# Kernel optimization log

Measured on AMD Instinct MI355X. Metric: run time of the kernel, lower is better.

## Reference

```python
import jax, jax.numpy as jnp
import numpy as np

EPS = 1e-5  # torch LayerNorm default
DT_RANK = 32  # ceil(d_model=512 / 16)


def layer_norm(x, g, b):
    mu = x.mean(-1, keepdims=True)
    var = x.var(-1, keepdims=True)
    return (x - mu) / jnp.sqrt(var + EPS) * g + b


def conv1d(x, w, b, pad):
    # x: (B, C, L), w: (O, I, K) -- torch Conv1d semantics
    y = jax.lax.conv_general_dilated(x, w, (1,), [(pad, pad)],
                                     dimension_numbers=('NCH', 'OIH', 'NCH'))
    return y + b[None, :, None]


def mamba(u, in_w, conv_w, conv_b, xproj_w, dt_w, dt_b, Alog, D, out_w, d_state, d_conv):
    # Faithful mamba_ssm Mamba block (no biases on in/x/out proj, RMS of official impl)
    Bsz, L, _ = u.shape
    xz = jnp.einsum('bld,ed->ble', u, in_w)          # (B, L, 2*Di)
    x, z = jnp.split(xz, 2, axis=-1)
    Di = x.shape[-1]
    # causal depthwise conv1d, truncated to L (padding=d_conv-1 on the left)
    xc = jax.lax.conv_general_dilated(x.transpose(0, 2, 1), conv_w[:, None, :], (1,),
                                      [(d_conv - 1, 0)],
                                      dimension_numbers=('NCH', 'OIH', 'NCH'),
                                      feature_group_count=Di)
    x = jax.nn.silu((xc + conv_b[None, :, None]).transpose(0, 2, 1))  # (B, L, Di)
    xdb = jnp.einsum('bld,ed->ble', x, xproj_w)       # (B, L, dt_rank + 2*N)
    dt = jax.nn.softplus(jnp.einsum('blr,dr->bld', xdb[..., :DT_RANK], dt_w) + dt_b)
    Bm = xdb[..., DT_RANK:DT_RANK + d_state]          # (B, L, N)
    Cm = xdb[..., DT_RANK + d_state:]                 # (B, L, N)
    A = -jnp.exp(Alog)                                # (Di, N)

    def step(h, ins):
        dt_t, x_t, B_t, C_t = ins                     # (B,Di),(B,Di),(B,N),(B,N)
        dA = jnp.exp(dt_t[..., None] * A)             # (B, Di, N)
        h = dA * h + (dt_t * x_t)[..., None] * B_t[:, None, :]
        y = (h * C_t[:, None, :]).sum(-1)             # (B, Di)
        return h, y

    h0 = jnp.zeros((Bsz, Di, d_state), u.dtype)
    xs = (dt.transpose(1, 0, 2), x.transpose(1, 0, 2),
          Bm.transpose(1, 0, 2), Cm.transpose(1, 0, 2))
    _, ys = jax.lax.scan(step, h0, xs)
    y = ys.transpose(1, 0, 2) + x * D                 # skip via D
    y = y * jax.nn.silu(z)
    return jnp.einsum('bld,od->blo', y, out_w)


def _forward(x, fe_w, fe_b, fe_ln_g, fe_ln_b, emb_ln_g, emb_ln_b,
             conv1_w, conv1_b, conv2_w, conv2_b,
             mf_in_w, mf_conv_w, mf_conv_b, mf_xproj_w, mf_dt_w, mf_dt_b, mf_Alog, mf_D, mf_out_w,
             mb_in_w, mb_conv_w, mb_conv_b, mb_xproj_w, mb_dt_w, mb_dt_b, mb_Alog, mb_D, mb_out_w,
             norm_g, norm_b, fc1_w, fc1_b, fc2_w, fc2_b):
    x = x.reshape(x.shape[0], 100, 23)
    # FrequencyEmbedding: rfft over a length-1 last dim == the signal itself; |.| then Linear+LN+ReLU
    id_mag = jnp.abs(x[..., :1])                      # (B, 100, 1)
    e = jax.nn.relu(layer_norm(id_mag @ fe_w.T + fe_b, fe_ln_g, fe_ln_b))
    id_embed = jax.nn.relu(layer_norm(e, emb_ln_g, emb_ln_b))  # outer LN+ReLU
    data = x[..., 1:].transpose(0, 2, 1)              # (B, 22, 100)
    f1 = jax.nn.relu(conv1d(data, conv1_w, conv1_b, 1))
    f2 = jax.nn.relu(conv1d(f1, conv2_w, conv2_b, 1)).transpose(0, 2, 1)  # (B,100,256)
    comb = jnp.concatenate([id_embed, f2], axis=-1)   # (B, 100, 512)
    fo = mamba(comb, mf_in_w, mf_conv_w, mf_conv_b, mf_xproj_w, mf_dt_w, mf_dt_b,
               mf_Alog, mf_D, mf_out_w, 16, 4)
    bo = mamba(comb[:, ::-1], mb_in_w, mb_conv_w, mb_conv_b, mb_xproj_w, mb_dt_w, mb_dt_b,
               mb_Alog, mb_D, mb_out_w, 8, 2)[:, ::-1]
    pooled = (fo + bo).max(axis=1)                    # (B, 512)
    pooled = layer_norm(pooled, norm_g, norm_b)       # self.norm (undefined in source; LN(512))
    h = jax.nn.relu(pooled @ fc1_w.T + fc1_b)
    return h @ fc2_w.T + fc2_b                        # (B, 4)


def setup_inputs() -> dict:
    key = jax.random.key(0)
    ks = iter(jax.random.split(key, 48))
    def n(shape, s=0.02):
        return jax.random.normal(next(ks), shape, jnp.float32) * s
    Di = 1024
    alog16 = jnp.log(jnp.tile(jnp.arange(1, 17, dtype=jnp.float32), (Di, 1)))
    alog8 = jnp.log(jnp.tile(jnp.arange(1, 9, dtype=jnp.float32), (Di, 1)))
    return {
        'x': jax.random.normal(next(ks), (512, 2300), jnp.float32),
        'fe_w': n((256, 1), 1.0), 'fe_b': jnp.zeros(256, jnp.float32),
        'fe_ln_g': jnp.ones(256, jnp.float32), 'fe_ln_b': jnp.zeros(256, jnp.float32),
        'emb_ln_g': jnp.ones(256, jnp.float32), 'emb_ln_b': jnp.zeros(256, jnp.float32),
        'conv1_w': n((128, 22, 3)), 'conv1_b': jnp.zeros(128, jnp.float32),
        'conv2_w': n((256, 128, 3)), 'conv2_b': jnp.zeros(256, jnp.float32),
        'mf_in_w': n((2 * Di, 512)), 'mf_conv_w': n((Di, 4)), 'mf_conv_b': jnp.zeros(Di, jnp.float32),
        'mf_xproj_w': n((32 + 2 * 16, Di)), 'mf_dt_w': n((Di, 32)), 'mf_dt_b': n((Di,), 0.1),
        'mf_Alog': alog16, 'mf_D': jnp.ones(Di, jnp.float32), 'mf_out_w': n((512, Di)),
        'mb_in_w': n((2 * Di, 512)), 'mb_conv_w': n((Di, 2)), 'mb_conv_b': jnp.zeros(Di, jnp.float32),
        'mb_xproj_w': n((32 + 2 * 8, Di)), 'mb_dt_w': n((Di, 32)), 'mb_dt_b': n((Di,), 0.1),
        'mb_Alog': alog8, 'mb_D': jnp.ones(Di, jnp.float32), 'mb_out_w': n((512, Di)),
        'norm_g': jnp.ones(512, jnp.float32), 'norm_b': jnp.zeros(512, jnp.float32),
        'fc1_w': n((128, 512)), 'fc1_b': jnp.zeros(128, jnp.float32),
        'fc2_w': n((4, 128)), 'fc2_b': jnp.zeros(4, jnp.float32),
    }


def reference(x, fe_w, fe_b, fe_ln_g, fe_ln_b, emb_ln_g, emb_ln_b,
              conv1_w, conv1_b, conv2_w, conv2_b,
              mf_in_w, mf_conv_w, mf_conv_b, mf_xproj_w, mf_dt_w, mf_dt_b, mf_Alog, mf_D, mf_out_w,
              mb_in_w, mb_conv_w, mb_conv_b, mb_xproj_w, mb_dt_w, mb_dt_b, mb_Alog, mb_D, mb_out_w,
              norm_g, norm_b, fc1_w, fc1_b, fc2_w, fc2_b):
    return _forward(x, fe_w, fe_b, fe_ln_g, fe_ln_b, emb_ln_g, emb_ln_b,
                    conv1_w, conv1_b, conv2_w, conv2_b,
                    mf_in_w, mf_conv_w, mf_conv_b, mf_xproj_w, mf_dt_w, mf_dt_b, mf_Alog, mf_D, mf_out_w,
                    mb_in_w, mb_conv_w, mb_conv_b, mb_xproj_w, mb_dt_w, mb_dt_b, mb_Alog, mb_D, mb_out_w,
                    norm_g, norm_b, fc1_w, fc1_b, fc2_w, fc2_b)
```

## Files before the change

kernel.cpp:

```cpp
#include <hip/hip_runtime.h>
#include <cstddef>
#include <cstdint>

#define BSZ 512
#define SEQ 100

typedef __bf16 bf16_t;
typedef __attribute__((ext_vector_type(8))) __bf16 bf16x8;
typedef __attribute__((ext_vector_type(4))) float f32x4;

__device__ __forceinline__ float sigmoidf_(float v){ return 1.f/(1.f + __expf(-v)); }
__device__ __forceinline__ float siluf_(float v){ return v * sigmoidf_(v); }
__device__ __forceinline__ float softplusf_(float v){ return (v > 20.f) ? v : __logf(1.f + __expf(v)); }

__global__ __launch_bounds__(256) void cvt_bf16_kernel(
    const float* __restrict__ src, bf16_t* __restrict__ dst, int n)
{
    int i = blockIdx.x*256 + threadIdx.x;
    if (i < n) dst[i] = (bf16_t)src[i];
}

__global__ __launch_bounds__(256) void prep_outw_kernel(
    const float* __restrict__ of, const float* __restrict__ ob, bf16_t* __restrict__ W)
{
// ... 172 lines not shown
    for (int i = 0; i < 4; ++i)
        #pragma unroll
        for (int j = 0; j < 4; ++j)
            acc[i][j] = (f32x4){0.f, 0.f, 0.f, 0.f};

    for (int k0 = 0; k0 < K; k0 += 64){
        __syncthreads();
        #pragma unroll
        for (int hh = 0; hh < 2; ++hh){
            bf16_t* Asb = hh ? As1 : As0;
            bf16_t* Wsb = hh ? Ws1 : Ws0;
            #pragma unroll
            for (int q = 0; q < 2; ++q){
                const int rt = w*32 + q*16 + rsub;
                const int lq = csub ^ ((rt >> 1) & 3);
                int ra = m0 + rt; ra = (ra < Mtot) ? ra : (Mtot - 1);
                const bf16_t* ga = A + (size_t)ra*lda + k0 + hh*32 + lq*8;
                __builtin_amdgcn_global_load_lds(
                    (const __attribute__((address_space(1))) void*)ga,
                    (__attribute__((address_space(3))) void*)&Asb[(w*32 + q*16)*32], 16, 0, 0);
                const bf16_t* gw = W + (size_t)(n0 + rt)*K + k0 + hh*32 + lq*8;
                __builtin_amdgcn_global_load_lds(
                    (const __attribute__((address_space(1))) void*)gw,
                    (__attribute__((address_space(3))) void*)&Wsb[(w*32 + q*16)*32], 16, 0, 0);
            }
        }
        __syncthreads();

        #pragma unroll
        for (int hh = 0; hh < 2; ++hh){
            bf16_t* Asb = hh ? As1 : As0;
            bf16_t* Wsb = hh ? Ws1 : Ws0;
            bf16x8 af[4], bfv[4];
            #pragma unroll
            for (int i = 0; i < 4; ++i){
                const int ra = wOffM + i*16 + col;
                af[i]  = *(const bf16x8*)&Asb[ra*32 + (quad ^ ((ra >> 1) & 3))*8];
                const int rb = wOffN + i*16 + col;
                bfv[i] = *(const bf16x8*)&Wsb[rb*32 + (quad ^ ((rb >> 1) & 3))*8];
            }
            #pragma unroll
            for (int i = 0; i < 4; ++i)
                #pragma unroll
                for (int j = 0; j < 4; ++j)
                    acc[i][j] = __builtin_amdgcn_mfma_f32_16x16x32_bf16(af[i], bfv[j], acc[i][j], 0, 0, 0);
        }
    }

    __syncthreads();
    #pragma unroll
    for (int i = 0; i < 4; ++i){
        const int row0 = wOffM + i*16 + quad*4;
        #pragma unroll
        for (int j = 0; j < 4; ++j){
            const int cT = wOffN + j*16 + col;
            #pragma unroll
            for (int r = 0; r < 4; ++r)
                smem[(row0 + r)*132 + cT] = (bf16_t)acc[i][j][r];
        }
    }
    __syncthreads();

    const int half = n0 >> 11, within = n0 & 2047;
    bf16_t* dstBase = ((within < 1024) ? xy : z) + half*1024 + (within & 1023);
    #pragma unroll
    for (int k = 0; k < 8; ++k){
        const int idx = t + k*256;
        const int row = idx >> 4;
        const int ch  = (idx & 15) * 8;
        const int gm = m0 + row;
        if (gm < Mtot)
            *(bf16x8*)&dstBase[(size_t)gm*2048 + ch] = *(const bf16x8*)&smem[row*132 + ch];
    }
}

__global__ __launch_bounds__(256) void gemm_out_kernel(
    const bf16_t* __restrict__ A, int Mtot,
    const bf16_t* __restrict__ W,
    float* __restrict__ C)
{
    __shared__ bf16_t As[2][128*32];
    __shared__ bf16_t Ws[2][128*32];
    const int t = threadIdx.x;
    const int lane = t & 63, w = t >> 6;
    const int m0 = blockIdx.x * 128, n0 = blockIdx.y * 128;
    const int rsub = lane >> 2, csub = lane & 3;
    const int col = lane & 15, quad = lane >> 4;
    const int wOffM = (w & 1) * 64, wOffN = (w >> 1) * 64;
    const int K = 2048;

    f32x4 acc[4][4];
    #pragma unroll
    for (int i = 0; i < 4; ++i)
        #pragma unroll
        for (int j = 0; j < 4; ++j)
            acc[i][j] = (f32x4){0.f, 0.f, 0.f, 0.f};

    for (int k0 = 0; k0 < K; k0 += 64){
        __syncthreads();
        #pragma unroll
        for (int hh = 0; hh < 2; ++hh){
            #pragma unroll
            for (int q = 0; q < 2; ++q){
                const int rt = w*32 + q*16 + rsub;
                const int lq = csub ^ ((rt >> 1) & 3);
                int ra = m0 + rt; ra = (ra < Mtot) ? ra : (Mtot - 1);
                const bf16_t* ga = A + (size_t)ra*K + k0 + hh*32 + lq*8;
                __builtin_amdgcn_global_load_lds(
                    (const __attribute__((address_space(1))) void*)ga,
                    (__attribute__((address_space(3))) void*)&As[hh][(w*32 + q*16)*32], 16, 0, 0);
                const bf16_t* gw = W + (size_t)(n0 + rt)*K + k0 + hh*32 + lq*8;
                __builtin_amdgcn_global_load_lds(
                    (const __attribute__((address_space(1))) void*)gw,
                    (__attribute__((address_space(3))) void*)&Ws[hh][(w*32 + q*16)*32], 16, 0, 0);
            }
        }
        __syncthreads();

        #pragma unroll
        for (int hh = 0; hh < 2; ++hh){
            bf16x8 af[4], bfv[4];
            #pragma unroll
            for (int i = 0; i < 4; ++i){
                const int ra = wOffM + i*16 + col;
                af[i]  = *(const bf16x8*)&As[hh][ra*32 + (quad ^ ((ra >> 1) & 3))*8];
                const int rb = wOffN + i*16 + col;
                bfv[i] = *(const bf16x8*)&Ws[hh][rb*32 + (quad ^ ((rb >> 1) & 3))*8];
            }
            #pragma unroll
            for (int i = 0; i < 4; ++i)
                #pragma unroll
                for (int j = 0; j < 4; ++j)
                    acc[i][j] = __builtin_amdgcn_mfma_f32_16x16x32_bf16(af[i], bfv[j], acc[i][j], 0, 0, 0);
        }
    }

    #pragma unroll
    for (int i = 0; i < 4; ++i){
        const int gmb = m0 + wOffM + i*16 + quad*4;
        #pragma unroll
        for (int j = 0; j < 4; ++j){
            const int gn = n0 + wOffN + j*16 + col;
            #pragma unroll
            for (int r = 0; r < 4; ++r){
                const int gm = gmb + r;
                if (gm < Mtot)
                    C[(size_t)gm*512 + gn] = acc[i][j][r];
            }
        }
    }
}

__global__ __launch_bounds__(256) void gemm_x_kernel(
    const bf16_t* __restrict__ xy,
    const bf16_t* __restrict__ Wf, const bf16_t* __restrict__ Wb,
    float* __restrict__ C)
{
    __shared__ bf16_t As[128*32];
    __shared__ bf16_t Ws[64*32];
    const int half = blockIdx.y;
    const bf16_t* A = xy + half*1024;
    const bf16_t* W = half ? Wb : Wf;
    const int N = half ? 48 : 64;
    const int t = threadIdx.x;
    const int lane = t & 63, w = t >> 6;
    const int m0 = blockIdx.x * 128;
    const int rsub = lane >> 2, csub = lane & 3;
    const int col = lane & 15, quad = lane >> 4;

    f32x4 acc[2][4];
    #pragma unroll
    for (int i = 0; i < 2; ++i)
        #pragma unroll
        for (int j = 0; j < 4; ++j)
            acc[i][j] = (f32x4){0.f, 0.f, 0.f, 0.f};

    for (int k0 = 0; k0 < 1024; k0 += 32){
        __syncthreads();
        #pragma unroll
        for (int q = 0; q < 2; ++q){
            const int rt = q*64 + w*16 + rsub;
            const int lq = csub ^ ((rt >> 1) & 3);
            const bf16_t* ga = A + (size_t)(m0 + rt)*2048 + k0 + lq*8;
            __builtin_amdgcn_global_load_lds(
                (const __attribute__((address_space(1))) void*)ga,
                (__attribute__((address_space(3))) void*)&As[(q*64 + w*16)*32], 16, 0, 0);
        }
        {
            const int rt = w*16 + rsub;
            const int lq = csub ^ ((rt >> 1) & 3);
            int rw = (rt < N) ? rt : (N - 1);
            const bf16_t* gw = W + (size_t)rw*1024 + k0 + lq*8;
            __builtin_amdgcn_global_load_lds(
                (const __attribute__((address_space(1))) void*)gw,
                (__attribute__((address_space(3))) void*)&Ws[(w*16)*32], 16, 0, 0);
        }
        __syncthreads();

        bf16x8 af[2], bfv[4];
        #pragma unroll
        for (int i = 0; i < 2; ++i){
            const int ra = w*32 + i*16 + col;
            af[i]  = *(const bf16x8*)&As[ra*32 + (quad ^ ((ra >> 1) & 3))*8];
        }
        #pragma unroll
        for (int j = 0; j < 4; ++j){
            const int rb = j*16 + col;
            bfv[j] = *(const bf16x8*)&Ws[rb*32 + (quad ^ ((rb >> 1) & 3))*8];
        }
        #pragma unroll
        for (int i = 0; i < 2; ++i)
            #pragma unroll
            for (int j = 0; j < 4; ++j)
                acc[i][j] = __builtin_amdgcn_mfma_f32_16x16x32_bf16(af[i], bfv[j], acc[i][j], 0, 0, 0);
    }

    #pragma unroll
    for (int i = 0; i < 2; ++i){
        const int gmb = m0 + w*32 + i*16 + quad*4;
        #pragma unroll
        for (int j = 0; j < 4; ++j){
            const int gn = j*16 + col;
            if (gn < N){
                #pragma unroll
                for (int r = 0; r < 4; ++r)
                    C[(size_t)(gmb + r)*128 + half*64 + gn] = acc[i][j][r];
            }
        }
    }
}

__global__ __launch_bounds__(256) void dt_kernel(
    const float* __restrict__ xdb,
    const float* __restrict__ dtwf, const float* __restrict__ dtbf,
    const float* __restrict__ dtwb, const float* __restrict__ dtbb,
    bf16_t* __restrict__ dtb)
{
    const int half = blockIdx.y >> 3;
    const int d = (blockIdx.y & 7)*128 + (threadIdx.x & 127);
    const int mslot = threadIdx.x >> 7;
    const int m0 = blockIdx.x * 16;
    __shared__ float sd[16*32];
    for (int i = threadIdx.x; i < 16*32; i += 256){
        int r = i >> 5, c = i & 31;
        sd[i] = xdb[(size_t)(m0 + r)*128 + half*64 + c];
    }
    const float* dw = half ? dtwb : dtwf;
    float w[32];
    #pragma unroll
    for (int r = 0; r < 32; ++r) w[r] = dw[d*32 + r];
    const float db = half ? dtbb[d] : dtbf[d];
    __syncthreads();
    #pragma unroll
    for (int i = 0; i < 8; ++i){
        const int row = mslot + i*2;
        const float* rp = &sd[row*32];
        float a = db;
        #pragma unroll
        for (int r = 0; r < 32; ++r) a += w[r]*rp[r];
        dtb[(size_t)(m0 + row)*2048 + half*1024 + d] = (bf16_t)softplusf_(a);
    }
}

template<int DC, bool REV>
__device__ __forceinline__ void conv_dev(bf16_t* base, const float* wsrc, float bias)
{
    float w[DC];
    #pragma unroll
    for (int k = 0; k < DC; ++k) w[k] = wsrc[k];
    float hist[DC-1];
    #pragma unroll
    for (int k = 0; k < DC-1; ++k) hist[k] = 0.f;
    const int step = REV ? -1 : 1;
    int l = REV ? (SEQ-1) : 0;
    for (int t0 = 0; t0 < SEQ; t0 += 10){
        float v[10];
        #pragma unroll
        for (int i = 0; i < 10; ++i) v[i] = (float)base[(size_t)(l + step*i)*2048];
        float o[10];
        #pragma unroll
        for (int i = 0; i < 10; ++i){
            float a = bias + w[DC-1]*v[i];
            #pragma unroll
            for (int j = 1; j < DC; ++j) a += w[DC-1-j]*hist[j-1];
            #pragma unroll
            for (int j = DC-2; j >= 1; --j) hist[j] = hist[j-1];
            hist[0] = v[i];
            o[i] = siluf_(a);
        }
        #pragma unroll
        for (int i = 0; i < 10; ++i)
            base[(size_t)(l + step*i)*2048] = (bf16_t)o[i];
        l += step*10;
    }
}

__global__ __launch_bounds__(256) void conv_silu_kernel(
    bf16_t* __restrict__ xy,
    const float* __restrict__ cwf, const float* __restrict__ cbf,
    const float* __restrict__ cwb, const float* __restrict__ cbb)
{
    const int gid = blockIdx.x*256 + threadIdx.x;
    const int b = gid >> 11, d2 = gid & 2047;
    const int half = d2 >> 10, d = d2 & 1023;
    bf16_t* base = xy + (size_t)b*SEQ*2048 + d2;
    if (half == 0) conv_dev<4, false>(base, cwf + d*4, cbf[d]);
    else           conv_dev<2, true >(base, cwb + d*2, cbb[d]);
}

template<int DS, bool REV, bool STRUCT>
__device__ __forceinline__ void scan_core(
    bf16_t* __restrict__ xybase, const bf16_t* __restrict__ zbase,
    const bf16_t* __restrict__ tbase, const float* __restrict__ sx,
    const float* __restrict__ Av, float Dd)
{
    float h[DS];
    #pragma unroll
    for (int s = 0; s < DS; ++s) h[s] = 0.f;
    const int step = REV ? -1 : 1;
    const float A0 = Av[0];
    int l = REV ? (SEQ-1) : 0;

    for (int t0 = 0; t0 < SEQ; t0 += 10){
        float xr[10], zr[10], tr[10];
        #pragma unroll
        for (int i = 0; i < 10; ++i){
            const size_t li = (size_t)(l + step*i);
            xr[i] = (float)xybase[li*2048];
            zr[i] = (float)zbase[li*2048];
            tr[i] = (float)tbase[li*2048];
        }
        #pragma unroll
        for (int i = 0; i < 10; ++i){
            const int li = l + step*i;
            const float4* sxl4 = (const float4*)&sx[li*2*DS];
            const float dtv = tr[i];
            const float dtx = dtv * xr[i];
            float yv = 0.f;
            if (STRUCT){
                const float r = __expf(dtv*A0);
                float rp = r;
                #pragma unroll
                for (int s4 = 0; s4 < DS/4; ++s4){
                    float4 Bv = sxl4[s4];
                    float4 Cv = sxl4[DS/4 + s4];
                    h[s4*4+0] = rp*h[s4*4+0] + dtx*Bv.x; yv += h[s4*4+0]*Cv.x; rp *= r;
                    h[s4*4+1] = rp*h[s4*4+1] + dtx*Bv.y; yv += h[s4*4+1]*Cv.y; rp *= r;
                    h[s4*4+2] = rp*h[s4*4+2] + dtx*Bv.z; yv += h[s4*4+2]*Cv.z; rp *= r;
                    h[s4*4+3] = rp*h[s4*4+3] + dtx*Bv.w; yv += h[s4*4+3]*Cv.w; rp *= r;
                }
            } else {
                #pragma unroll
                for (int s4 = 0; s4 < DS/4; ++s4){
                    float4 Bv = sxl4[s4];
                    float4 Cv = sxl4[DS/4 + s4];
                    h[s4*4+0] = __expf(dtv*Av[s4*4+0])*h[s4*4+0] + dtx*Bv.x; yv += h[s4*4+0]*Cv.x;
                    h[s4*4+1] = __expf(dtv*Av[s4*4+1])*h[s4*4+1] + dtx*Bv.y; yv += h[s4*4+1]*Cv.y;
                    h[s4*4+2] = __expf(dtv*Av[s4*4+2])*h[s4*4+2] + dtx*Bv.z; yv += h[s4*4+2]*Cv.z;
                    h[s4*4+3] = __expf(dtv*Av[s4*4+3])*h[s4*4+3] + dtx*Bv.w; yv += h[s4*4+3]*Cv.w;
                }
            }
            yv += xr[i]*Dd;
            yv *= siluf_(zr[i]);
            xybase[(size_t)li*2048] = (bf16_t)yv;
        }
        l += step*10;
    }
}

template<int DS, bool REV>
__device__ __forceinline__ void scan_dev(
    bf16_t* __restrict__ xybase, const bf16_t* __restrict__ zbase,
    const bf16_t* __restrict__ tbase, const float* __restrict__ sx,
    const float* __restrict__ Arow, float Dd)
{
    float Av[DS];
    #pragma unroll
    for (int s = 0; s < DS; ++s) Av[s] = -__expf(Arow[s]);
    bool structured = true;
    #pragma unroll
    for (int s = 1; s < DS; ++s)
        structured = structured && (fabsf(Av[s] - (float)(s+1)*Av[0]) <= 1e-4f*(float)(s+1));
    if (structured) scan_core<DS, REV, true >(xybase, zbase, tbase, sx, Av, Dd);
    else            scan_core<DS, REV, false>(xybase, zbase, tbase, sx, Av, Dd);
}

__global__ __launch_bounds__(256) void scan_kernel(
    bf16_t* __restrict__ xy, const bf16_t* __restrict__ z,
    const bf16_t* __restrict__ dtb, const float* __restrict__ xdb,
    const float* __restrict__ Alogf, const float* __restrict__ Dpf,
    const float* __restrict__ Alogb, const float* __restrict__ Dpb)
{
    const int b = blockIdx.x >> 3, s8 = blockIdx.x & 7;
    const int t = threadIdx.x;
    __shared__ float sxF[SEQ*32];
    __shared__ float sxB[SEQ*16];
    const float4* src = (const float4*)(xdb + (size_t)b*SEQ*128);

    {
        float4* dstF = (float4*)sxF;
        for (int i = t; i < SEQ*8; i += 256){
            int row = i >> 3, c = i & 7;
            dstF[row*8 + c] = src[row*32 + 8 + c];
        }
        float4* dstB = (float4*)sxB;
        for (int i = t; i < SEQ*4; i += 256){
            int row = i >> 2, c = i & 3;
            dstB[row*4 + c] = src[row*32 + 24 + c];
        }
    }
    __syncthreads();

    if (t < 128){
        const int d = s8*128 + t;
        const size_t off = (size_t)b*SEQ*2048 + d;
        scan_dev<16, false>(xy + off, z + off, dtb + off, sxF, Alogf + d*16, Dpf[d]);
    } else {
        const int d = s8*128 + (t - 128);
        const size_t off = (size_t)b*SEQ*2048 + 1024 + d;
        scan_dev<8, true>(xy + off, z + off, dtb + off, sxB, Alogb + d*8, Dpb[d]);
    }
}

__global__ __launch_bounds__(256) void head_kernel(
    const float* __restrict__ acc,
    const float* __restrict__ ng, const float* __restrict__ nb,
    const float* __restrict__ w1, const float* __restrict__ b1,
    const float* __restrict__ w2, const float* __restrict__ b2,
    float* __restrict__ out)
{
    const int b = blockIdx.x, t = threadIdx.x;
    __shared__ float4 sm4[256];
    __shared__ float sp[512];
    __shared__ float sh2[256];
    __shared__ float sh[128];
    __shared__ float red1[4], red2[4];
    const float* base = acc + (size_t)b*SEQ*512;

    {
        const int c4 = t & 127, lh = t >> 7;
        float4 m = make_float4(-3.4e38f, -3.4e38f, -3.4e38f, -3.4e38f);
        for (int l = lh*50; l < lh*50 + 50; ++l){
            float4 v = ((const float4*)(base + (size_t)l*512))[c4];
            m.x = fmaxf(m.x, v.x); m.y = fmaxf(m.y, v.y);
            m.z = fmaxf(m.z, v.z); m.w = fmaxf(m.w, v.w);
        }
        sm4[t] = m;
    }
    __syncthreads();
    if (t < 128){
        float4 a = sm4[t], c = sm4[t + 128];
        ((float4*)sp)[t] = make_float4(fmaxf(a.x,c.x), fmaxf(a.y,c.y),
                                       fmaxf(a.z,c.z), fmaxf(a.w,c.w));
    }
    __syncthreads();

    float s1 = 0.f, s2 = 0.f;
    for (int o = t; o < 512; o += 256){ float v = sp[o]; s1 += v; s2 += v*v; }
    #pragma unroll
    for (int off = 32; off > 0; off >>= 1){ s1 += __shfl_xor(s1, off); s2 += __shfl_xor(s2, off); }
    const int wv = t >> 6, lane = t & 63;
    if (lane == 0){ red1[wv] = s1; red2[wv] = s2; }
    __syncthreads();
    if (t == 0){
        float a = 0.f, c = 0.f;
        for (int i = 0; i < 4; ++i){ a += red1[i]; c += red2[i]; }
        float mean = a * (1.f/512.f);
        float var = c * (1.f/512.f) - mean*mean;
        red1[0] = mean; red2[0] = rsqrtf(var + 1e-5f);
    }
    __syncthreads();
    const float mean = red1[0], rstd = red2[0];
    for (int o = t; o < 512; o += 256) sp[o] = (sp[o]-mean)*rstd*ng[o] + nb[o];
    __syncthreads();

    {
        const int o = t & 127, half = t >> 7;
        const float4* wrow = (const float4*)(w1 + (size_t)o*512 + half*256);
        const float4* sp4 = (const float4*)sp + half*64;
        float s = 0.f;
        #pragma unroll 8
        for (int j = 0; j < 64; ++j){
            float4 a = sp4[j], wq = wrow[j];
            s += a.x*wq.x + a.y*wq.y + a.z*wq.z + a.w*wq.w;
        }
        sh2[t] = s;
    }
    __syncthreads();
    if (t < 128) sh[t] = fmaxf(sh2[t] + sh2[t + 128] + b1[t], 0.f);
    __syncthreads();
    if (t < 4){
        float a = b2[t];
        for (int j = 0; j < 128; ++j) a += sh[j]*w2[t*128 + j];
        out[b*4 + t] = a;
    }
}

extern "C" void kernel_launch(void* const* d_in, const int* in_sizes, int n_in,
                              void* d_out, int out_size, void* d_ws, size_t ws_size,
                              hipStream_t stream)
{
    (void)in_sizes; (void)n_in; (void)out_size;
    const float* x        = (const float*)d_in[0];
    const float* fe_w     = (const float*)d_in[1];
    const float* fe_b     = (const float*)d_in[2];
    const float* fe_ln_g  = (const float*)d_in[3];
    const float* fe_ln_b  = (const float*)d_in[4];
    const float* emb_ln_g = (const float*)d_in[5];
    const float* emb_ln_b = (const float*)d_in[6];
    const float* conv1_w  = (const float*)d_in[7];
    const float* conv1_b  = (const float*)d_in[8];
    const float* conv2_w  = (const float*)d_in[9];
    const float* conv2_b  = (const float*)d_in[10];
    const float* mf_in_w  = (const float*)d_in[11];
    const float* mf_conv_w= (const float*)d_in[12];
    const float* mf_conv_b= (const float*)d_in[13];
    const float* mf_xproj = (const float*)d_in[14];
    const float* mf_dt_w  = (const float*)d_in[15];
    const float* mf_dt_b  = (const float*)d_in[16];
    const float* mf_Alog  = (const float*)d_in[17];
    const float* mf_D     = (const float*)d_in[18];
    const float* mf_out_w = (const float*)d_in[19];
    const float* mb_in_w  = (const float*)d_in[20];
    const float* mb_conv_w= (const float*)d_in[21];
    const float* mb_conv_b= (const float*)d_in[22];
    const float* mb_xproj = (const float*)d_in[23];
    const float* mb_dt_w  = (const float*)d_in[24];
    const float* mb_dt_b  = (const float*)d_in[25];
    const float* mb_Alog  = (const float*)d_in[26];
    const float* mb_D     = (const float*)d_in[27];
    const float* mb_out_w = (const float*)d_in[28];
    const float* norm_g   = (const float*)d_in[29];
    const float* norm_b   = (const float*)d_in[30];
    const float* fc1_w    = (const float*)d_in[31];
    const float* fc1_b    = (const float*)d_in[32];
    const float* fc2_w    = (const float*)d_in[33];
    const float* fc2_b    = (const float*)d_in[34];
    float* out = (float*)d_out;

    char* p = (char*)d_ws;
    bf16_t* w_in   = (bf16_t*)p; p += (size_t)4096*512*sizeof(bf16_t);
    bf16_t* w_out  = (bf16_t*)p; p += (size_t)512*2048*sizeof(bf16_t);
    bf16_t* w_xpf  = (bf16_t*)p; p += (size_t)64*1024*sizeof(bf16_t);
    bf16_t* w_xpb  = (bf16_t*)p; p += (size_t)48*1024*sizeof(bf16_t);
    bf16_t* W1p    = (bf16_t*)p; p += (size_t)128*96*sizeof(bf16_t);
    bf16_t* W2p    = (bf16_t*)p; p += (size_t)256*384*sizeof(bf16_t);
    bf16_t* comb_all = (bf16_t*)p; p += (size_t)BSZ*SEQ*512*sizeof(bf16_t);
    const size_t fixed_bytes = (size_t)(p - (char*)d_ws);

    const size_t per_b = (size_t)SEQ * (2048*2 + 2048*2 + 2048*2 + 128*4);
    const size_t budget = (ws_size > fixed_bytes) ? (ws_size - fixed_bytes) : 0;
    int Bc = BSZ;
    while (Bc > 64 && (size_t)Bc * per_b > budget) Bc >>= 1;
    const int nch = BSZ / Bc;
    const int M = Bc * SEQ;

    bf16_t* F0pad = (bf16_t*)p;
    bf16_t* F1pad = F0pad + (size_t)BSZ*102*32;
    bf16_t* xy   = (bf16_t*)p;               p += (size_t)M*2048*sizeof(bf16_t);
    bf16_t* z    = (bf16_t*)p;               p += (size_t)M*2048*sizeof(bf16_t);
    bf16_t* dtb  = (bf16_t*)p;               p += (size_t)M*2048*sizeof(bf16_t);
    float*  xdb  = (float*)p;
    float*  accb = (float*)dtb;

    cvt_bf16_kernel<<<(2048*512+255)/256, 256, 0, stream>>>(mf_in_w, w_in, 2048*512);
    cvt_bf16_kernel<<<(2048*512+255)/256, 256, 0, stream>>>(mb_in_w, w_in + (size_t)2048*512, 2048*512);
    prep_outw_kernel<<<(512*2048+255)/256, 256, 0, stream>>>(mf_out_w, mb_out_w, w_out);
    cvt_bf16_kernel<<<(64*1024+255)/256,  256, 0, stream>>>(mf_xproj, w_xpf, 64*1024);
    cvt_bf16_kernel<<<(48*1024+255)/256,  256, 0, stream>>>(mb_xproj, w_xpb, 48*1024);
    prep_convw_kernel<<<(256*384+255)/256, 256, 0, stream>>>(conv1_w, conv2_w, W1p, W2p);

    fe0_kernel<<<BSZ, 256, 0, stream>>>(x, fe_w, fe_b, fe_ln_g, fe_ln_b,
        emb_ln_g, emb_ln_b, comb_all, F0pad, F1pad);
    gemm_conv_kernel<<<dim3(1, 1, BSZ), 256, 0, stream>>>(
        F0pad, 32, 102*32, W1p, 96, 128, conv1_b, F1pad, 128, 102, 1, 0, SEQ);
    gemm_conv_kernel<<<dim3(1, 2, BSZ), 256, 0, stream>>>(
        F1pad, 128, 102*128, W2p, 384, 256, conv2_b, comb_all, 512, 100, 0, 256, SEQ);

    const int gm128 = M / 128;

    for (int c = 0; c < nch; ++c){
        const size_t b0 = (size_t)c * Bc;
        const bf16_t* comb = comb_all + b0*SEQ*512;

        gemm_in_kernel<<<dim3(gm128, 32), 256, 0, stream>>>(comb, 512, M, w_in, 512, xy, z);
        conv_silu_kernel<<<Bc*2048/256, 256, 0, stream>>>(xy, mf_conv_w, mf_conv_b,
                                                          mb_conv_w, mb_conv_b);
        gemm_x_kernel<<<dim3(gm128, 2), 256, 0, stream>>>(xy, w_xpf, w_xpb, xdb);
        dt_kernel<<<dim3(M/16, 16), 256, 0, stream>>>(xdb, mf_dt_w, mf_dt_b,
                                                      mb_dt_w, mb_dt_b, dtb);
        scan_kernel<<<Bc*8, 256, 0, stream>>>(xy, z, dtb, xdb,
                                              mf_Alog, mf_D, mb_Alog, mb_D);
        gemm_out_kernel<<<dim3(gm128, 4), 256, 0, stream>>>(xy, M, w_out, accb);
        head_kernel<<<Bc, 256, 0, stream>>>(accb, norm_g, norm_b, fc1_w, fc1_b,
                                            fc2_w, fc2_b, out + b0*4);
    }
}
```

Measured before the change: 1.528 ms.

## Double-buffer global loads in conv and scan, split max-pool from head

The conv and scan loops now use ping-pong register buffers, so the next block of 10 timesteps is loaded while the current block is computed, hiding global load latency. The structured scan also splits the y accumulation into four partial sums and computes decay powers with a shorter dependency chain. Max-pooling moves out of the head kernel into a separate pool kernel with more blocks, and its output reuses the xdb buffer. This adds register pressure, an extra kernel launch, and a dependency on xdb being free at that point.

```diff
diff --git a/kernel.cpp b/kernel.cpp
--- a/kernel.cpp
+++ b/kernel.cpp
@@ -458,6 +458,24 @@
     }
 }
 
+template<int DC>
+__device__ __forceinline__ void conv_blk10(
+    float* __restrict__ hist, const float* __restrict__ w, float bias,
+    const bf16_t* v, bf16_t* base, int l, int step)
+{
+    #pragma unroll
+    for (int i = 0; i < 10; ++i){
+        const float vi = (float)v[i];
+        float a = bias + w[DC-1]*vi;
+        #pragma unroll
+        for (int j = 1; j < DC; ++j) a += w[DC-1-j]*hist[j-1];
+        #pragma unroll
+        for (int j = DC-2; j >= 1; --j) hist[j] = hist[j-1];
+        hist[0] = vi;
+        base[(size_t)(l + step*i)*2048] = (bf16_t)siluf_(a);
+    }
+}
+
 template<int DC, bool REV>
 __device__ __forceinline__ void conv_dev(bf16_t* base, const float* wsrc, float bias)
 {
@@ -469,24 +487,26 @@
     for (int k = 0; k < DC-1; ++k) hist[k] = 0.f;
     const int step = REV ? -1 : 1;
     int l = REV ? (SEQ-1) : 0;
-    for (int t0 = 0; t0 < SEQ; t0 += 10){
-        float v[10];
-        #pragma unroll
-        for (int i = 0; i < 10; ++i) v[i] = (float)base[(size_t)(l + step*i)*2048];
-        float o[10];
-        #pragma unroll
-        for (int i = 0; i < 10; ++i){
-            float a = bias + w[DC-1]*v[i];
-            #pragma unroll
-            for (int j = 1; j < DC; ++j) a += w[DC-1-j]*hist[j-1];
-            #pragma unroll
-            for (int j = DC-2; j >= 1; --j) hist[j] = hist[j-1];
-            hist[0] = v[i];
-            o[i] = siluf_(a);
-        }
-        #pragma unroll
-        for (int i = 0; i < 10; ++i)
-            base[(size_t)(l + step*i)*2048] = (bf16_t)o[i];
+
+    bf16_t vA[10], vB[10];
+    #pragma unroll
+    for (int i = 0; i < 10; ++i) vA[i] = base[(size_t)(l + step*i)*2048];
+
+    #pragma unroll 1
+    for (int pair = 0; pair < 5; ++pair){
+        {
+            const int lb = l + step*10;
+            #pragma unroll
+            for (int i = 0; i < 10; ++i) vB[i] = base[(size_t)(lb + step*i)*2048];
+        }
+        conv_blk10<DC>(hist, w, bias, vA, base, l, step);
+        l += step*10;
+        if (pair < 4){
+            const int lb = l + step*10;
+            #pragma unroll
+            for (int i = 0; i < 10; ++i) vA[i] = base[(size_t)(lb + step*i)*2048];
+        }
+        conv_blk10<DC>(hist, w, bias, vB, base, l, step);
         l += step*10;
     }
 }
@@ -504,6 +524,53 @@
     else           conv_dev<2, true >(base, cwb + d*2, cbb[d]);
 }
 
+template<int DS, bool STRUCT>
+__device__ __forceinline__ void scan_blk10(
+    float* __restrict__ h,
+    const bf16_t* xr, const bf16_t* zr, const bf16_t* tr,
+    const float* __restrict__ sx, const float* __restrict__ Av,
+    float A0, float Dd, bf16_t* __restrict__ xybase, int l, int step)
+{
+    #pragma unroll
+    for (int i = 0; i < 10; ++i){
+        const int li = l + step*i;
+        const float4* sxl4 = (const float4*)&sx[li*2*DS];
+        const float dtv = (float)tr[i];
+        const float xv  = (float)xr[i];
+        const float dtx = dtv * xv;
+        float yv0 = 0.f, yv1 = 0.f, yv2 = 0.f, yv3 = 0.f;
+        if (STRUCT){
+            const float r  = __expf(dtv*A0);
+            const float r2 = r*r;
+            float rb = r;
+            #pragma unroll
+            for (int g = 0; g < DS/4; ++g){
+                float4 Bv = sxl4[g];
+                float4 Cv = sxl4[DS/4 + g];
+                const float p0 = rb, p1 = rb*r, p2 = rb*r2, p3 = p1*r2;
+                h[g*4+0] = p0*h[g*4+0] + dtx*Bv.x; yv0 += h[g*4+0]*Cv.x;
+                h[g*4+1] = p1*h[g*4+1] + dtx*Bv.y; yv1 += h[g*4+1]*Cv.y;
+                h[g*4+2] = p2*h[g*4+2] + dtx*Bv.z; yv2 += h[g*4+2]*Cv.z;
+                h[g*4+3] = p3*h[g*4+3] + dtx*Bv.w; yv3 += h[g*4+3]*Cv.w;
+                rb = p3*r;
+            }
+        } else {
+            #pragma unroll
+            for (int g = 0; g < DS/4; ++g){
+                float4 Bv = sxl4[g];
+                float4 Cv = sxl4[DS/4 + g];
+                h[g*4+0] = __expf(dtv*Av[g*4+0])*h[g*4+0] + dtx*Bv.x; yv0 += h[g*4+0]*Cv.x;
+                h[g*4+1] = __expf(dtv*Av[g*4+1])*h[g*4+1] + dtx*Bv.y; yv1 += h[g*4+1]*Cv.y;
+                h[g*4+2] = __expf(dtv*Av[g*4+2])*h[g*4+2] + dtx*Bv.z; yv2 += h[g*4+2]*Cv.z;
+                h[g*4+3] = __expf(dtv*Av[g*4+3])*h[g*4+3] + dtx*Bv.w; yv3 += h[g*4+3]*Cv.w;
+            }
+        }
+        float yv = (yv0 + yv1) + (yv2 + yv3) + xv*Dd;
+        yv *= siluf_((float)zr[i]);
+        xybase[(size_t)li*2048] = (bf16_t)yv;
+    }
+}
+
 template<int DS, bool REV, bool STRUCT>
 __device__ __forceinline__ void scan_core(
     bf16_t* __restrict__ xybase, const bf16_t* __restrict__ zbase,
@@ -517,49 +584,41 @@
     const float A0 = Av[0];
     int l = REV ? (SEQ-1) : 0;
 
-    for (int t0 = 0; t0 < SEQ; t0 += 10){
-        float xr[10], zr[10], tr[10];
-        #pragma unroll
-        for (int i = 0; i < 10; ++i){
-            const size_t li = (size_t)(l + step*i);
-            xr[i] = (float)xybase[li*2048];
-            zr[i] = (float)zbase[li*2048];
-            tr[i] = (float)tbase[li*2048];
-        }
-        #pragma unroll
-        for (int i = 0; i < 10; ++i){
-            const int li = l + step*i;
-            const float4* sxl4 = (const float4*)&sx[li*2*DS];
-            const float dtv = tr[i];
-            const float dtx = dtv * xr[i];
-            float yv = 0.f;
-            if (STRUCT){
-                const float r = __expf(dtv*A0);
-                float rp = r;
-                #pragma unroll
-                for (int s4 = 0; s4 < DS/4; ++s4){
-                    float4 Bv = sxl4[s4];
-                    float4 Cv = sxl4[DS/4 + s4];
-                    h[s4*4+0] = rp*h[s4*4+0] + dtx*Bv.x; yv += h[s4*4+0]*Cv.x; rp *= r;
-                    h[s4*4+1] = rp*h[s4*4+1] + dtx*Bv.y; yv += h[s4*4+1]*Cv.y; rp *= r;
-                    h[s4*4+2] = rp*h[s4*4+2] + dtx*Bv.z; yv += h[s4*4+2]*Cv.z; rp *= r;
-                    h[s4*4+3] = rp*h[s4*4+3] + dtx*Bv.w; yv += h[s4*4+3]*Cv.w; rp *= r;
-                }
-            } else {
-                #pragma unroll
-                for (int s4 = 0; s4 < DS/4; ++s4){
-                    float4 Bv = sxl4[s4];
-                    float4 Cv = sxl4[DS/4 + s4];
-                    h[s4*4+0] = __expf(dtv*Av[s4*4+0])*h[s4*4+0] + dtx*Bv.x; yv += h[s4*4+0]*Cv.x;
-                    h[s4*4+1] = __expf(dtv*Av[s4*4+1])*h[s4*4+1] + dtx*Bv.y; yv += h[s4*4+1]*Cv.y;
-                    h[s4*4+2] = __expf(dtv*Av[s4*4+2])*h[s4*4+2] + dtx*Bv.z; yv += h[s4*4+2]*Cv.z;
-                    h[s4*4+3] = __expf(dtv*Av[s4*4+3])*h[s4*4+3] + dtx*Bv.w; yv += h[s4*4+3]*Cv.w;
-                }
-            }
-            yv += xr[i]*Dd;
-            yv *= siluf_(zr[i]);
-            xybase[(size_t)li*2048] = (bf16_t)yv;
-        }
+    bf16_t xA[10], zA[10], tA[10], xB[10], zB[10], tB[10];
+
+    #pragma unroll
+    for (int i = 0; i < 10; ++i){
+        const size_t li = (size_t)(l + step*i);
+        xA[i] = xybase[li*2048];
+        zA[i] = zbase[li*2048];
+        tA[i] = tbase[li*2048];
+    }
+
+    #pragma unroll 1
+    for (int pair = 0; pair < 5; ++pair){
+        {
+            const int lb = l + step*10;
+            #pragma unroll
+            for (int i = 0; i < 10; ++i){
+                const size_t li = (size_t)(lb + step*i);
+                xB[i] = xybase[li*2048];
+                zB[i] = zbase[li*2048];
+                tB[i] = tbase[li*2048];
+            }
+        }
+        scan_blk10<DS, STRUCT>(h, xA, zA, tA, sx, Av, A0, Dd, xybase, l, step);
+        l += step*10;
+        if (pair < 4){
+            const int lb = l + step*10;
+            #pragma unroll
+            for (int i = 0; i < 10; ++i){
+                const size_t li = (size_t)(lb + step*i);
+                xA[i] = xybase[li*2048];
+                zA[i] = zbase[li*2048];
+                tA[i] = tbase[li*2048];
+            }
+        }
+        scan_blk10<DS, STRUCT>(h, xB, zB, tB, sx, Av, A0, Dd, xybase, l, step);
         l += step*10;
     }
 }
@@ -618,41 +677,43 @@
     }
 }
 
+__global__ __launch_bounds__(256) void pool_kernel(
+    const float* __restrict__ acc,
+    float* __restrict__ pooled)
+{
+    const int b = blockIdx.x, y = blockIdx.y;
+    const int c = y*128 + (threadIdx.x & 127);
+    const int half = threadIdx.x >> 7;
+    const float* base = acc + (size_t)b*SEQ*512 + c;
+    float m = -3.4e38f;
+    #pragma unroll 5
+    for (int l = half*50; l < half*50 + 50; ++l)
+        m = fmaxf(m, base[(size_t)l*512]);
+    __shared__ float sm[256];
+    sm[threadIdx.x] = m;
+    __syncthreads();
+    if (half == 0)
+        pooled[(size_t)b*512 + c] = fmaxf(sm[threadIdx.x], sm[threadIdx.x + 128]);
+}
+
 __global__ __launch_bounds__(256) void head_kernel(
-    const float* __restrict__ acc,
+    const float* __restrict__ pooled,
     const float* __restrict__ ng, const float* __restrict__ nb,
     const float* __restrict__ w1, const float* __restrict__ b1,
     const float* __restrict__ w2, const float* __restrict__ b2,
     float* __restrict__ out)
 {
     const int b = blockIdx.x, t = threadIdx.x;
-    __shared__ float4 sm4[256];
     __shared__ float sp[512];
     __shared__ float sh2[256];
     __shared__ float sh[128];
     __shared__ float red1[4], red2[4];
-    const float* base = acc + (size_t)b*SEQ*512;
-
-    {
-        const int c4 = t & 127, lh = t >> 7;
-        float4 m = make_float4(-3.4e38f, -3.4e38f, -3.4e38f, -3.4e38f);
-        for (int l = lh*50; l < lh*50 + 50; ++l){
-            float4 v = ((const float4*)(base + (size_t)l*512))[c4];
-            m.x = fmaxf(m.x, v.x); m.y = fmaxf(m.y, v.y);
-            m.z = fmaxf(m.z, v.z); m.w = fmaxf(m.w, v.w);
-        }
-        sm4[t] = m;
-    }
-    __syncthreads();
-    if (t < 128){
-        float4 a = sm4[t], c = sm4[t + 128];
-        ((float4*)sp)[t] = make_float4(fmaxf(a.x,c.x), fmaxf(a.y,c.y),
-                                       fmaxf(a.z,c.z), fmaxf(a.w,c.w));
-    }
-    __syncthreads();
 
     float s1 = 0.f, s2 = 0.f;
-    for (int o = t; o < 512; o += 256){ float v = sp[o]; s1 += v; s2 += v*v; }
+    for (int o = t; o < 512; o += 256){
+        float v = pooled[(size_t)b*512 + o];
+        sp[o] = v; s1 += v; s2 += v*v;
+    }
     #pragma unroll
     for (int off = 32; off > 0; off >>= 1){ s1 += __shfl_xor(s1, off); s2 += __shfl_xor(s2, off); }
     const int wv = t >> 6, lane = t & 63;
@@ -788,7 +849,8 @@
         scan_kernel<<<Bc*8, 256, 0, stream>>>(xy, z, dtb, xdb,
                                               mf_Alog, mf_D, mb_Alog, mb_D);
         gemm_out_kernel<<<dim3(gm128, 4), 256, 0, stream>>>(xy, M, w_out, accb);
-        head_kernel<<<Bc, 256, 0, stream>>>(accb, norm_g, norm_b, fc1_w, fc1_b,
+        pool_kernel<<<dim3(Bc, 4), 256, 0, stream>>>(accb, xdb);
+        head_kernel<<<Bc, 256, 0, stream>>>(xdb, norm_g, norm_b, fc1_w, fc1_b,
                                             fc2_w, fc2_b, out + b0*4);
     }
 }
```

Measured after the change: 1.635 ms. +7.0%, slower.

## Parallelize conv over time chunks, split scan states across lanes, separate pooling

Applied to the files above, without the earlier changes.

The depthwise conv becomes out-of-place, with each thread handling a 10-step time chunk, which exposes more threads than one thread walking the whole sequence. The selective scan now spreads each channel's state across 4 lanes and combines the outputs with shuffles, giving 4x more blocks. This drops the structured-A power-trick path in favour of one exp per state. Max-pooling moves into its own kernel, and buffers are re-aliased so conv output, dt, and the accumulator live in different scratch regions. The costs are more exp work per step, the shuffle reductions, and one extra kernel launch.

```diff
diff --git a/kernel.cpp b/kernel.cpp
--- a/kernel.cpp
+++ b/kernel.cpp
@@ -348,14 +348,14 @@
 }
 
 __global__ __launch_bounds__(256) void gemm_x_kernel(
-    const bf16_t* __restrict__ xy,
+    const bf16_t* __restrict__ xc,
     const bf16_t* __restrict__ Wf, const bf16_t* __restrict__ Wb,
     float* __restrict__ C)
 {
     __shared__ bf16_t As[128*32];
     __shared__ bf16_t Ws[64*32];
     const int half = blockIdx.y;
-    const bf16_t* A = xy + half*1024;
+    const bf16_t* A = xc + half*1024;
     const bf16_t* W = half ? Wb : Wf;
     const int N = half ? 48 : 64;
     const int t = threadIdx.x;
@@ -430,7 +430,7 @@
     const float* __restrict__ xdb,
     const float* __restrict__ dtwf, const float* __restrict__ dtbf,
     const float* __restrict__ dtwb, const float* __restrict__ dtbb,
-    bf16_t* __restrict__ dtb)
+    bf16_t* __restrict__ dto)
 {
     const int half = blockIdx.y >> 3;
     const int d = (blockIdx.y & 7)*128 + (threadIdx.x & 127);
@@ -454,205 +454,192 @@
         float a = db;
         #pragma unroll
         for (int r = 0; r < 32; ++r) a += w[r]*rp[r];
-        dtb[(size_t)(m0 + row)*2048 + half*1024 + d] = (bf16_t)softplusf_(a);
-    }
-}
-
-template<int DC, bool REV>
-__device__ __forceinline__ void conv_dev(bf16_t* base, const float* wsrc, float bias)
-{
-    float w[DC];
-    #pragma unroll
-    for (int k = 0; k < DC; ++k) w[k] = wsrc[k];
-    float hist[DC-1];
-    #pragma unroll
-    for (int k = 0; k < DC-1; ++k) hist[k] = 0.f;
+        dto[(size_t)(m0 + row)*2048 + half*1024 + d] = (bf16_t)softplusf_(a);
+    }
+}
+
+__global__ __launch_bounds__(256) void conv_silu_kernel(
+    const bf16_t* __restrict__ xin,
+    bf16_t* __restrict__ xout,
+    const float* __restrict__ cwf, const float* __restrict__ cbf,
+    const float* __restrict__ cwb, const float* __restrict__ cbb)
+{
+    const int gid = blockIdx.x*256 + threadIdx.x;
+    const int d2 = gid & 2047;
+    const int rest = gid >> 11;
+    const int b = rest / 10;
+    const int g = rest - b*10;
+    const int l0 = g*10;
+    const int half = d2 >> 10, d = d2 & 1023;
+    const bf16_t* in = xin + (size_t)b*SEQ*2048 + d2;
+    bf16_t* outp = xout + (size_t)b*SEQ*2048 + d2;
+
+    if (half == 0){
+        const float w0 = cwf[d*4], w1 = cwf[d*4+1], w2 = cwf[d*4+2], w3 = cwf[d*4+3];
+        const float bias = cbf[d];
+        float v[13];
+        #pragma unroll
+        for (int i = 0; i < 13; ++i){
+            const int l = l0 - 3 + i;
+            v[i] = (l >= 0) ? (float)in[(size_t)l*2048] : 0.f;
+        }
+        #pragma unroll
+        for (int i = 0; i < 10; ++i){
+            const float a = bias + w0*v[i] + w1*v[i+1] + w2*v[i+2] + w3*v[i+3];
+            outp[(size_t)(l0+i)*2048] = (bf16_t)siluf_(a);
+        }
+    } else {
+        const float w0 = cwb[d*2], w1 = cwb[d*2+1];
+        const float bias = cbb[d];
+        float v[11];
+        #pragma unroll
+        for (int i = 0; i < 11; ++i){
+            const int l = l0 + i;
+            v[i] = (l < SEQ) ? (float)in[(size_t)l*2048] : 0.f;
+        }
+        #pragma unroll
+        for (int i = 0; i < 10; ++i){
+            const float a = bias + w1*v[i] + w0*v[i+1];
+            outp[(size_t)(l0+i)*2048] = (bf16_t)siluf_(a);
+        }
+    }
+}
+
+template<int DSS, int ROW, bool REV>
+__device__ __forceinline__ void scan2_core(
+    bf16_t* __restrict__ xcb,
+    const bf16_t* __restrict__ tb,
+    const bf16_t* __restrict__ zb,
+    const float* __restrict__ sxB,
+    const float* __restrict__ sxC,
+    const float* __restrict__ Av, float Dd, bool wr)
+{
+    float h[DSS];
+    #pragma unroll
+    for (int j = 0; j < DSS; ++j) h[j] = 0.f;
     const int step = REV ? -1 : 1;
     int l = REV ? (SEQ-1) : 0;
-    for (int t0 = 0; t0 < SEQ; t0 += 10){
-        float v[10];
-        #pragma unroll
-        for (int i = 0; i < 10; ++i) v[i] = (float)base[(size_t)(l + step*i)*2048];
-        float o[10];
-        #pragma unroll
-        for (int i = 0; i < 10; ++i){
-            float a = bias + w[DC-1]*v[i];
-            #pragma unroll
-            for (int j = 1; j < DC; ++j) a += w[DC-1-j]*hist[j-1];
-            #pragma unroll
-            for (int j = DC-2; j >= 1; --j) hist[j] = hist[j-1];
-            hist[0] = v[i];
-            o[i] = siluf_(a);
-        }
-        #pragma unroll
-        for (int i = 0; i < 10; ++i)
-            base[(size_t)(l + step*i)*2048] = (bf16_t)o[i];
-        l += step*10;
-    }
-}
-
-__global__ __launch_bounds__(256) void conv_silu_kernel(
-    bf16_t* __restrict__ xy,
-    const float* __restrict__ cwf, const float* __restrict__ cbf,
-    const float* __restrict__ cwb, const float* __restrict__ cbb)
-{
-    const int gid = blockIdx.x*256 + threadIdx.x;
-    const int b = gid >> 11, d2 = gid & 2047;
-    const int half = d2 >> 10, d = d2 & 1023;
-    bf16_t* base = xy + (size_t)b*SEQ*2048 + d2;
-    if (half == 0) conv_dev<4, false>(base, cwf + d*4, cbf[d]);
-    else           conv_dev<2, true >(base, cwb + d*2, cbb[d]);
-}
-
-template<int DS, bool REV, bool STRUCT>
-__device__ __forceinline__ void scan_core(
-    bf16_t* __restrict__ xybase, const bf16_t* __restrict__ zbase,
-    const bf16_t* __restrict__ tbase, const float* __restrict__ sx,
-    const float* __restrict__ Av, float Dd)
-{
-    float h[DS];
-    #pragma unroll
-    for (int s = 0; s < DS; ++s) h[s] = 0.f;
-    const int step = REV ? -1 : 1;
-    const float A0 = Av[0];
-    int l = REV ? (SEQ-1) : 0;
-
-    for (int t0 = 0; t0 < SEQ; t0 += 10){
+
+    #pragma unroll 1
+    for (int blk = 0; blk < 10; ++blk){
         float xr[10], zr[10], tr[10];
         #pragma unroll
         for (int i = 0; i < 10; ++i){
             const size_t li = (size_t)(l + step*i);
-            xr[i] = (float)xybase[li*2048];
-            zr[i] = (float)zbase[li*2048];
-            tr[i] = (float)tbase[li*2048];
+            xr[i] = (float)xcb[li*2048];
+            zr[i] = (float)zb[li*2048];
+            tr[i] = (float)tb[li*2048];
         }
         #pragma unroll
         for (int i = 0; i < 10; ++i){
             const int li = l + step*i;
-            const float4* sxl4 = (const float4*)&sx[li*2*DS];
             const float dtv = tr[i];
             const float dtx = dtv * xr[i];
+            const float* Bp = &sxB[li*ROW];
+            const float* Cp = &sxC[li*ROW];
             float yv = 0.f;
-            if (STRUCT){
-                const float r = __expf(dtv*A0);
-                float rp = r;
-                #pragma unroll
-                for (int s4 = 0; s4 < DS/4; ++s4){
-                    float4 Bv = sxl4[s4];
-                    float4 Cv = sxl4[DS/4 + s4];
-                    h[s4*4+0] = rp*h[s4*4+0] + dtx*Bv.x; yv += h[s4*4+0]*Cv.x; rp *= r;
-                    h[s4*4+1] = rp*h[s4*4+1] + dtx*Bv.y; yv += h[s4*4+1]*Cv.y; rp *= r;
-                    h[s4*4+2] = rp*h[s4*4+2] + dtx*Bv.z; yv += h[s4*4+2]*Cv.z; rp *= r;
-                    h[s4*4+3] = rp*h[s4*4+3] + dtx*Bv.w; yv += h[s4*4+3]*Cv.w; rp *= r;
-                }
-            } else {
-                #pragma unroll
-                for (int s4 = 0; s4 < DS/4; ++s4){
-                    float4 Bv = sxl4[s4];
-                    float4 Cv = sxl4[DS/4 + s4];
-                    h[s4*4+0] = __expf(dtv*Av[s4*4+0])*h[s4*4+0] + dtx*Bv.x; yv += h[s4*4+0]*Cv.x;
-                    h[s4*4+1] = __expf(dtv*Av[s4*4+1])*h[s4*4+1] + dtx*Bv.y; yv += h[s4*4+1]*Cv.y;
-                    h[s4*4+2] = __expf(dtv*Av[s4*4+2])*h[s4*4+2] + dtx*Bv.z; yv += h[s4*4+2]*Cv.z;
-                    h[s4*4+3] = __expf(dtv*Av[s4*4+3])*h[s4*4+3] + dtx*Bv.w; yv += h[s4*4+3]*Cv.w;
-                }
+            #pragma unroll
+            for (int j = 0; j < DSS; ++j){
+                h[j] = __expf(dtv*Av[j])*h[j] + dtx*Bp[j];
+                yv += h[j]*Cp[j];
             }
+            yv += __shfl_xor(yv, 1);
+            yv += __shfl_xor(yv, 2);
             yv += xr[i]*Dd;
             yv *= siluf_(zr[i]);
-            xybase[(size_t)li*2048] = (bf16_t)yv;
+            if (wr) xcb[(size_t)li*2048] = (bf16_t)yv;
         }
         l += step*10;
     }
 }
 
-template<int DS, bool REV>
-__device__ __forceinline__ void scan_dev(
-    bf16_t* __restrict__ xybase, const bf16_t* __restrict__ zbase,
-    const bf16_t* __restrict__ tbase, const float* __restrict__ sx,
-    const float* __restrict__ Arow, float Dd)
-{
-    float Av[DS];
-    #pragma unroll
-    for (int s = 0; s < DS; ++s) Av[s] = -__expf(Arow[s]);
-    bool structured = true;
-    #pragma unroll
-    for (int s = 1; s < DS; ++s)
-        structured = structured && (fabsf(Av[s] - (float)(s+1)*Av[0]) <= 1e-4f*(float)(s+1));
-    if (structured) scan_core<DS, REV, true >(xybase, zbase, tbase, sx, Av, Dd);
-    else            scan_core<DS, REV, false>(xybase, zbase, tbase, sx, Av, Dd);
-}
-
 __global__ __launch_bounds__(256) void scan_kernel(
-    bf16_t* __restrict__ xy, const bf16_t* __restrict__ z,
-    const bf16_t* __restrict__ dtb, const float* __restrict__ xdb,
+    bf16_t* __restrict__ xc,
+    const bf16_t* __restrict__ dtv,
+    const bf16_t* __restrict__ z,
+    const float* __restrict__ xdb,
     const float* __restrict__ Alogf, const float* __restrict__ Dpf,
     const float* __restrict__ Alogb, const float* __restrict__ Dpb)
 {
-    const int b = blockIdx.x >> 3, s8 = blockIdx.x & 7;
+    const int b = blockIdx.x >> 5, k = blockIdx.x & 31;
     const int t = threadIdx.x;
-    __shared__ float sxF[SEQ*32];
-    __shared__ float sxB[SEQ*16];
+    const int sub = t & 3, chl = t >> 2;
+    const bool fwd = (k < 16);
+
+    __shared__ float sx[SEQ*32];
     const float4* src = (const float4*)(xdb + (size_t)b*SEQ*128);
-
-    {
-        float4* dstF = (float4*)sxF;
+    if (fwd){
+        float4* dst = (float4*)sx;
         for (int i = t; i < SEQ*8; i += 256){
             int row = i >> 3, c = i & 7;
-            dstF[row*8 + c] = src[row*32 + 8 + c];
-        }
-        float4* dstB = (float4*)sxB;
+            dst[row*8 + c] = src[row*32 + 8 + c];
+        }
+    } else {
+        float4* dst = (float4*)sx;
         for (int i = t; i < SEQ*4; i += 256){
             int row = i >> 2, c = i & 3;
-            dstB[row*4 + c] = src[row*32 + 24 + c];
-        }
-    }
-    __syncthreads();
-
-    if (t < 128){
-        const int d = s8*128 + t;
+            dst[row*4 + c] = src[row*32 + 24 + c];
+        }
+    }
+    __syncthreads();
+
+    const bool wr = (sub == 0);
+    if (fwd){
+        const int d = k*64 + chl;
         const size_t off = (size_t)b*SEQ*2048 + d;
-        scan_dev<16, false>(xy + off, z + off, dtb + off, sxF, Alogf + d*16, Dpf[d]);
+        float Av[4];
+        #pragma unroll
+        for (int j = 0; j < 4; ++j) Av[j] = -__expf(Alogf[d*16 + sub*4 + j]);
+        scan2_core<4, 32, false>(xc + off, dtv + off, z + off,
+                                 sx + sub*4, sx + 16 + sub*4, Av, Dpf[d], wr);
     } else {
-        const int d = s8*128 + (t - 128);
+        const int d = (k - 16)*64 + chl;
         const size_t off = (size_t)b*SEQ*2048 + 1024 + d;
-        scan_dev<8, true>(xy + off, z + off, dtb + off, sxB, Alogb + d*8, Dpb[d]);
-    }
+        float Av[2];
+        #pragma unroll
+        for (int j = 0; j < 2; ++j) Av[j] = -__expf(Alogb[d*8 + sub*2 + j]);
+        scan2_core<2, 16, true>(xc + off, dtv + off, z + off,
+                                sx + sub*2, sx + 8 + sub*2, Av, Dpb[d], wr);
+    }
+}
+
+__global__ __launch_bounds__(256) void pool_kernel(
+    const float* __restrict__ acc,
+    float* __restrict__ pooled)
+{
+    const int b = blockIdx.x, y = blockIdx.y;
+    const int c = y*128 + (threadIdx.x & 127);
+    const int half = threadIdx.x >> 7;
+    const float* base = acc + (size_t)b*SEQ*512 + c;
+    float m = -3.4e38f;
+    #pragma unroll 5
+    for (int l = half*50; l < half*50 + 50; ++l)
+        m = fmaxf(m, base[(size_t)l*512]);
+    __shared__ float sm[256];
+    sm[threadIdx.x] = m;
+    __syncthreads();
+    if (half == 0)
+        pooled[(size_t)b*512 + c] = fmaxf(sm[threadIdx.x], sm[threadIdx.x + 128]);
 }
 
 __global__ __launch_bounds__(256) void head_kernel(
-    const float* __restrict__ acc,
+    const float* __restrict__ pooled,
     const float* __restrict__ ng, const float* __restrict__ nb,
     const float* __restrict__ w1, const float* __restrict__ b1,
     const float* __restrict__ w2, const float* __restrict__ b2,
     float* __restrict__ out)
 {
     const int b = blockIdx.x, t = threadIdx.x;
-    __shared__ float4 sm4[256];
     __shared__ float sp[512];
     __shared__ float sh2[256];
     __shared__ float sh[128];
     __shared__ float red1[4], red2[4];
-    const float* base = acc + (size_t)b*SEQ*512;
-
-    {
-        const int c4 = t & 127, lh = t >> 7;
-        float4 m = make_float4(-3.4e38f, -3.4e38f, -3.4e38f, -3.4e38f);
-        for (int l = lh*50; l < lh*50 + 50; ++l){
-            float4 v = ((const float4*)(base + (size_t)l*512))[c4];
-            m.x = fmaxf(m.x, v.x); m.y = fmaxf(m.y, v.y);
-            m.z = fmaxf(m.z, v.z); m.w = fmaxf(m.w, v.w);
-        }
-        sm4[t] = m;
-    }
-    __syncthreads();
-    if (t < 128){
-        float4 a = sm4[t], c = sm4[t + 128];
-        ((float4*)sp)[t] = make_float4(fmaxf(a.x,c.x), fmaxf(a.y,c.y),
-                                       fmaxf(a.z,c.z), fmaxf(a.w,c.w));
-    }
-    __syncthreads();
 
     float s1 = 0.f, s2 = 0.f;
-    for (int o = t; o < 512; o += 256){ float v = sp[o]; s1 += v; s2 += v*v; }
+    for (int o = t; o < 512; o += 256){
+        float v = pooled[(size_t)b*512 + o];
+        sp[o] = v; s1 += v; s2 += v*v;
+    }
     #pragma unroll
     for (int off = 32; off > 0; off >>= 1){ s1 += __shfl_xor(s1, off); s2 += __shfl_xor(s2, off); }
     const int wv = t >> 6, lane = t & 63;
@@ -757,7 +744,7 @@
     bf16_t* z    = (bf16_t*)p;               p += (size_t)M*2048*sizeof(bf16_t);
     bf16_t* dtb  = (bf16_t*)p;               p += (size_t)M*2048*sizeof(bf16_t);
     float*  xdb  = (float*)p;
-    float*  accb = (float*)dtb;
+    float*  accb = (float*)xy;
 
     cvt_bf16_kernel<<<(2048*512+255)/256, 256, 0, stream>>>(mf_in_w, w_in, 2048*512);
     cvt_bf16_kernel<<<(2048*512+255)/256, 256, 0, stream>>>(mb_in_w, w_in + (size_t)2048*512, 2048*512);
@@ -780,15 +767,16 @@
         const bf16_t* comb = comb_all + b0*SEQ*512;
 
         gemm_in_kernel<<<dim3(gm128, 32), 256, 0, stream>>>(comb, 512, M, w_in, 512, xy, z);
-        conv_silu_kernel<<<Bc*2048/256, 256, 0, stream>>>(xy, mf_conv_w, mf_conv_b,
-                                                          mb_conv_w, mb_conv_b);
-        gemm_x_kernel<<<dim3(gm128, 2), 256, 0, stream>>>(xy, w_xpf, w_xpb, xdb);
+        conv_silu_kernel<<<Bc*80, 256, 0, stream>>>(xy, dtb, mf_conv_w, mf_conv_b,
+                                                    mb_conv_w, mb_conv_b);
+        gemm_x_kernel<<<dim3(gm128, 2), 256, 0, stream>>>(dtb, w_xpf, w_xpb, xdb);
         dt_kernel<<<dim3(M/16, 16), 256, 0, stream>>>(xdb, mf_dt_w, mf_dt_b,
-                                                      mb_dt_w, mb_dt_b, dtb);
-        scan_kernel<<<Bc*8, 256, 0, stream>>>(xy, z, dtb, xdb,
-                                              mf_Alog, mf_D, mb_Alog, mb_D);
-        gemm_out_kernel<<<dim3(gm128, 4), 256, 0, stream>>>(xy, M, w_out, accb);
-        head_kernel<<<Bc, 256, 0, stream>>>(accb, norm_g, norm_b, fc1_w, fc1_b,
+                                                      mb_dt_w, mb_dt_b, xy);
+        scan_kernel<<<Bc*32, 256, 0, stream>>>(dtb, xy, z, xdb,
+                                               mf_Alog, mf_D, mb_Alog, mb_D);
+        gemm_out_kernel<<<dim3(gm128, 4), 256, 0, stream>>>(dtb, M, w_out, accb);
+        pool_kernel<<<dim3(Bc, 4), 256, 0, stream>>>(accb, xdb);
+        head_kernel<<<Bc, 256, 0, stream>>>(xdb, norm_g, norm_b, fc1_w, fc1_b,
                                             fc2_w, fc2_b, out + b0*4);
     }
 }
```

New measurement: 1.791 ms. 17.2% more time.
